# Performance work log

Measured on AMD Instinct MI355X. Metric: run time of the kernel, lower is better.

## Reference

```python
import jax, jax.numpy as jnp
import numpy as np

N = 100000      # nodes
E = 1600000     # edges (before self-loops)
F_IN = 256      # input features
H = 8           # heads, layer 1
FH = 8          # features per head, layer 1
C = 64          # n_classes (layer 2 out, heads=1)
SLOPE = 0.2     # leaky relu negative slope


def setup_inputs() -> dict:
    key = jax.random.key(0)
    ks = jax.random.split(key, 12)
    x = jax.random.normal(ks[0], (N, F_IN), jnp.float32)
    edge_index = jax.random.randint(ks[1], (2, E), 0, N, dtype=jnp.int32)
    # scalar edge weights in [0.5, 1.5) so the (1 - 1/w) correction is well-behaved
    edge_weight = jax.random.uniform(ks[2], (E,), jnp.float32, 0.5, 1.5)
    W1 = jax.random.normal(ks[3], (F_IN, H * FH), jnp.float32) / np.sqrt(F_IN)
    att_src1 = jax.random.normal(ks[4], (H, FH), jnp.float32) * 0.1
    att_dst1 = jax.random.normal(ks[5], (H, FH), jnp.float32) * 0.1
    b1 = jnp.zeros((H * FH,), jnp.float32)
    W2 = jax.random.normal(ks[6], (H * FH, C), jnp.float32) / np.sqrt(H * FH)
    att_src2 = jax.random.normal(ks[7], (1, C), jnp.float32) * 0.1
    att_dst2 = jax.random.normal(ks[8], (1, C), jnp.float32) * 0.1
    b2 = jnp.zeros((C,), jnp.float32)
    return {"x": x, "edge_index": edge_index, "edge_weight": edge_weight,
            "W1": W1, "att_src1": att_src1, "att_dst1": att_dst1, "b1": b1,
            "W2": W2, "att_src2": att_src2, "att_dst2": att_dst2, "b2": b2}


def _gat_layer(x, src, dst, ew, W, a_src, a_dst, b, heads, fph, concat):
    n = x.shape[0]
    h = (x @ W).reshape(n, heads, fph)                      # [N,H,F]
    al_src = jnp.sum(h * a_src, axis=-1)                    # [N,H]
    al_dst = jnp.sum(h * a_dst, axis=-1)                    # [N,H]
    alpha = jax.nn.leaky_relu(al_src[src] + al_dst[dst], SLOPE)  # [E,H]
    alpha = alpha + (1.0 - 1.0 / ew)[:, None]               # scalar edge-weight correction
    # segment softmax over destination nodes
    m = jax.ops.segment_max(alpha, dst, num_segments=n)
    e = jnp.exp(alpha - m[dst])
    s = jax.ops.segment_sum(e, dst, num_segments=n)
    alpha = e / (s[dst] + 1e-16)                            # [E,H]
    msg = h[src] * alpha[:, :, None]                        # [E,H,F]
    out = jax.ops.segment_sum(msg, dst, num_segments=n)     # [N,H,F]
    out = out.reshape(n, heads * fph) if concat else out.mean(axis=1)
    return out + b


def reference(x, edge_index, edge_weight, W1, att_src1, att_dst1, b1,
              W2, att_src2, att_dst2, b2):
    n = x.shape[0]
    loops = jnp.arange(n, dtype=edge_index.dtype)
    src = jnp.concatenate([edge_index[0], loops])
    dst = jnp.concatenate([edge_index[1], loops])
    ew = jnp.concatenate([edge_weight, jnp.ones((n,), edge_weight.dtype)])  # fill_value=1.0
    # dropout layers are identity in eval mode
    h = _gat_layer(x, src, dst, ew, W1, att_src1, att_dst1, b1, H, FH, concat=True)
    h = jax.nn.elu(h)
    out = _gat_layer(h, src, dst, ew, W2, att_src2, att_dst2, b2, 1, C, concat=False)
    return out
```

## Files before the change

kernel.cpp:

```cpp
#include <hip/hip_runtime.h>
#include <math.h>

#define NNODES 100000
#define NEDGES 1600000
#define EATOT  1700000
#define FIN    256
#define C1     64
#define NH     8
#define C2     64
#define SLOPE  0.2f
#define LOG2E  1.4426950408889634f
#define QSCALE 8192.0f

#define NBKT  391
#define BCAP  5120
#define EPB_A 4096
#define NBLK_A 416

#define NT1 3125
#define NT2 1563
#define GGRID 512

typedef __attribute__((ext_vector_type(8))) short short8;
typedef __attribute__((ext_vector_type(4))) float f32x4;

__device__ __forceinline__ unsigned short f2bf(float f){
  unsigned u = __float_as_uint(f);
  unsigned r = (u + 0x7FFFu + ((u >> 16) & 1u)) >> 16;
  return (unsigned short)r;
}

__device__ __forceinline__ void splitw_body(const float* __restrict__ W,
                                            short* __restrict__ th, short* __restrict__ tl,
                                            int K, int idx){
  int k = idx >> 6, c = idx & 63;
  float w = W[idx];
  unsigned int b = __float_as_uint(w);
  unsigned short h = (unsigned short)(b >> 16);
  float hf = __uint_as_float(b & 0xffff0000u);
  float rem = w - hf;
  unsigned short lo = (unsigned short)(__float_as_uint(rem) >> 16);
  th[c * K + k] = (short)h;
  tl[c * K + k] = (short)lo;
}

__global__ void k_pre(const float* __restrict__ W1, short* __restrict__ w1h,
                      short* __restrict__ w1l, const float* __restrict__ W2,
                      short* __restrict__ w2h, short* __restrict__ w2l,
                      int* __restrict__ gcount){
  int b = blockIdx.x, t = threadIdx.x;
  if (b < 64){
    splitw_body(W1, w1h, w1l, FIN, b * 256 + t);
  } else if (b < 80){
    splitw_body(W2, w2h, w2l, C1, (b - 64) * 256 + t);
  } else {
    for (int i = t; i < NBKT; i += 256) gcount[i] = 0;
  }
}

__global__ __launch_bounds__(256) void k_bucketA(
    const int* __restrict__ ei, const float* __restrict__ ew,
    int* __restrict__ gcount, uint2* __restrict__ brec){
  __shared__ int cnt[NBKT];
  __shared__ int base[NBKT];
  int t = threadIdx.x;
  for (int i = t; i < NBKT; i += 256) cnt[i] = 0;
  __syncthreads();
  int e0 = blockIdx.x * EPB_A;
  int e1 = e0 + EPB_A; if (e1 > EATOT) e1 = EATOT;

  int dv[16]; unsigned pv[16];
  #pragma unroll
  for (int i = 0; i < 16; ++i){
    int e = e0 + t + i * 256;
    dv[i] = -1;
    if (e < e1){
      int s, d; float corr;
      if (e < NEDGES){ s = ei[e]; d = ei[NEDGES + e]; corr = 1.0f - 1.0f / ew[e]; }
      else { s = e - NEDGES; d = s; corr = 0.0f; }
      int q = __float2int_rn(corr * (LOG2E * QSCALE));
      dv[i] = d;
      pv[i] = ((unsigned)q << 17) | (unsigned)s;
      atomicAdd(&cnt[d >> 8], 1);
    }
  }
  __syncthreads();
  for (int i = t; i < NBKT; i += 256){
    int c = cnt[i];
    base[i] = c ? atomicAdd(&gcount[i], c) : 0;
    cnt[i] = 0;
  }
  __syncthreads();
  #pragma unroll
  for (int i = 0; i < 16; ++i){
    if (dv[i] >= 0){
      int bkt = dv[i] >> 8;
      int rel = base[bkt] + atomicAdd(&cnt[bkt], 1);
      brec[(size_t)bkt * BCAP + rel] = make_uint2((unsigned)dv[i], pv[i]);
    }
  }
}

__global__ void k_bucketS(const int* __restrict__ gcount, int* __restrict__ gbase,
                          int* __restrict__ rowptr){
  __shared__ int sh[512];
  int t = threadIdx.x;
  int v = (t < NBKT) ? gcount[t] : 0;
  sh[t] = v; __syncthreads();
  for (int off = 1; off < 512; off <<= 1){
    int y = (t >= off) ? sh[t - off] : 0;
    __syncthreads();
    sh[t] += y;
    __syncthreads();
  }
  if (t < NBKT) gbase[t] = sh[t] - v;
  if (t == 0) rowptr[NNODES] = EATOT;
}

__global__ __launch_bounds__(256, 2) void k_bg1(
    const uint2* __restrict__ brec, const int* __restrict__ gcount,
    const int* __restrict__ gbase, int* __restrict__ rowptr, int* __restrict__ rec,
    const float* __restrict__ X, const short* __restrict__ Bth,
    const short* __restrict__ Btl, const float* __restrict__ asrc,
    const float* __restrict__ adst, unsigned short* __restrict__ Hout,
    float* __restrict__ alsrc, float* __restrict__ aldst)
{
  __shared__ float xbuf[2][32 * 256];

  if (blockIdx.x < NBKT){
    int* hist  = (int*)&xbuf[0][0];
    int* scanb = hist + 256;
    int* excl  = scanb + 256;
    int* cur   = excl + 256;
    int bkt = blockIdx.x;
    int t = threadIdx.x;
    int n0 = bkt << 8;
    int cnt = gcount[bkt];
    int gb = gbase[bkt];
    hist[t] = 0;
    __syncthreads();
    const uint2* breg = brec + (size_t)bkt * BCAP;
    for (int j = t; j < cnt; j += 256)
      atomicAdd(&hist[breg[j].x & 255u], 1);
    __syncthreads();
    int h = hist[t];
    scanb[t] = h;
    __syncthreads();
    for (int off = 1; off < 256; off <<= 1){
      int y = (t >= off) ? scanb[t - off] : 0;
      __syncthreads();
      scanb[t] += y;
      __syncthreads();
    }
    int ex = scanb[t] - h;
    excl[t] = ex;
    cur[t] = 0;
    if (n0 + t < NNODES) rowptr[n0 + t] = gb + ex;
    __syncthreads();
    for (int j = t; j < cnt; j += 256){
      uint2 r = breg[j];
      int dl = (int)(r.x & 255u);
      int pos = gb + excl[dl] + atomicAdd(&cur[dl], 1);
      rec[pos] = (int)r.y;
    }
    return;
  }

  const int lane = threadIdx.x & 63;
  const int wave = threadIdx.x >> 6;
  const int l15 = lane & 15;
  const int kg = lane >> 4;
  const int cp = wave & 1;
  const int rh = wave >> 1;
  const int rl = rh * 16 + l15;
  const int rs = rl & 7;

  short8 bh[8][2], bl[8][2];
  #pragma unroll
  for (int ks = 0; ks < 8; ++ks){
    #pragma unroll
    for (int cc = 0; cc < 2; ++cc){
      unsigned boff = (unsigned)((cp * 2 + cc) * 16 + l15) * FIN + ks * 32 + kg * 8;
      bh[ks][cc] = *(const short8*)&Bth[boff];
      bl[ks][cc] = *(const short8*)&Btl[boff];
    }
  }
  float ascv[2], adcv[2];
  #pragma unroll
  for (int cc = 0; cc < 2; ++cc){
    ascv[cc] = asrc[(cp * 2 + cc) * 16 + l15] * LOG2E;
    adcv[cc] = adst[(cp * 2 + cc) * 16 + l15] * LOG2E;
  }

  const int t0 = blockIdx.x - NBKT;
  #pragma unroll
  for (int t = 0; t < 8; ++t){
    int r = wave * 8 + t;
    unsigned u = (unsigned)(lane ^ (r & 7));
    __builtin_amdgcn_global_load_lds(
        (const unsigned int*)(X + (size_t)(t0 * 32 + r) * FIN + u * 4),
        (unsigned int*)&xbuf[0][r * 256], 16, 0, 0);
  }

  int cur = 0;
  for (int ti = t0; ti < NT1; ti += GGRID){
    __syncthreads();
    int nxt = ti + GGRID;
    if (nxt < NT1){
      #pragma unroll
      for (int t = 0; t < 8; ++t){
        int r = wave * 8 + t;
        unsigned u = (unsigned)(lane ^ (r & 7));
        __builtin_amdgcn_global_load_lds(
            (const unsigned int*)(X + (size_t)(nxt * 32 + r) * FIN + u * 4),
            (unsigned int*)&xbuf[cur ^ 1][r * 256], 16, 0, 0);
      }
    }

    f32x4 acc[2] = {f32x4{0,0,0,0}, f32x4{0,0,0,0}};
    #pragma unroll
    for (int ks = 0; ks < 8; ++ks){
      int k0 = ks * 32 + kg * 8;
      unsigned U = (unsigned)(k0 >> 2);
      float4 xa = *(const float4*)&xbuf[cur][rl * 256 + ((U ^ rs) << 2)];
      float4 xb = *(const float4*)&xbuf[cur][rl * 256 + (((U + 1) ^ rs) << 2)];
      float xs[8] = {xa.x, xa.y, xa.z, xa.w, xb.x, xb.y, xb.z, xb.w};
      short8 ah, al;
      #pragma unroll
      for (int j = 0; j < 8; ++j){
        unsigned u = __float_as_uint(xs[j]);
        ah[j] = (short)(u >> 16);
        float hf = __uint_as_float(u & 0xffff0000u);
        al[j] = (short)(__float_as_uint(xs[j] - hf) >> 16);
      }
      #pragma unroll
      for (int cc = 0; cc < 2; ++cc){
        acc[cc] = __builtin_amdgcn_mfma_f32_16x16x32_bf16(ah, bh[ks][cc], acc[cc], 0, 0, 0);
        acc[cc] = __builtin_amdgcn_mfma_f32_16x16x32_bf16(ah, bl[ks][cc], acc[cc], 0, 0, 0);
        acc[cc] = __builtin_amdgcn_mfma_f32_16x16x32_bf16(al, bh[ks][cc], acc[cc], 0, 0, 0);
      }
    }

    int rowg = ti * 32 + rh * 16 + kg * 4;
    #pragma unroll
    for (int cc = 0; cc < 2; ++cc){
      #pragma unroll
      for (int reg = 0; reg < 4; ++reg)
        Hout[(size_t)(rowg + reg) * 64 + (cp * 2 + cc) * 16 + l15] = f2bf(acc[cc][reg]);
    }
    #pragma unroll
    for (int reg = 0; reg < 4; ++reg){
      int r = rowg + reg;
      #pragma unroll
      for (int cc = 0; cc < 2; ++cc){
        float ps = acc[cc][reg] * ascv[cc];
        float pd = acc[cc][reg] * adcv[cc];
        ps += __shfl_xor(ps, 1, 64); ps += __shfl_xor(ps, 2, 64); ps += __shfl_xor(ps, 4, 64);
        pd += __shfl_xor(pd, 1, 64); pd += __shfl_xor(pd, 2, 64); pd += __shfl_xor(pd, 4, 64);
        if ((l15 & 7) == 0){
          int head = (cp * 2 + cc) * 2 + (l15 >> 3);
          alsrc[r * NH + head] = ps;
          aldst[r * NH + head] = pd;
        }
      }
    }
    cur ^= 1;
  }
}

__global__ __launch_bounds__(256, 2) void k_gemm2(
    const unsigned short* __restrict__ Ah, const unsigned short* __restrict__ Al,
    const short* __restrict__ Bth, const short* __restrict__ Btl,
    const float* __restrict__ asrc, const float* __restrict__ adst,
    unsigned short* __restrict__ Hout, float* __restrict__ alsrc,
    float* __restrict__ aldst)
{
  __shared__ unsigned short abuf[2][2][64 * 64];
  const int lane = threadIdx.x & 63;
  const int wave = threadIdx.x >> 6;
  const int l15 = lane & 15;
  const int kg = lane >> 4;
  const int rl = wave * 16 + l15;
  const int rs = rl & 7;

  short8 bh[2][4], bl[2][4];
  #pragma unroll
  for (int ks = 0; ks < 2; ++ks){
    #pragma unroll
    for (int c = 0; c < 4; ++c){
      unsigned boff = (unsigned)(c * 16 + l15) * C1 + ks * 32 + kg * 8;
      bh[ks][c] = *(const short8*)&Bth[boff];
      bl[ks][c] = *(const short8*)&Btl[boff];
    }
  }
  float ascv[4], adcv[4];
  #pragma unroll
  for (int c = 0; c < 4; ++c){
    ascv[c] = asrc[c * 16 + l15] * LOG2E;
    adcv[c] = adst[c * 16 + l15] * LOG2E;
  }

  const int t0 = blockIdx.x;
  auto stage = [&](int buf, int tile){
    #pragma unroll
    for (int j = 0; j < 4; ++j){
      int q = wave * 4 + j;
      int p = q >> 3, rb = q & 7;
      int r = rb * 8 + (lane >> 3);
      int rg = tile * 64 + r; if (rg > NNODES - 1) rg = NNODES - 1;
      unsigned u = (unsigned)((lane & 7) ^ (lane >> 3));
      const unsigned short* src = (p ? Al : Ah) + (size_t)rg * 64 + u * 8;
      __builtin_amdgcn_global_load_lds(
          (const unsigned int*)src,
          (unsigned int*)&abuf[buf][p][rb * 512], 16, 0, 0);
    }
  };
  stage(0, t0);

  int cur = 0;
  for (int ti = t0; ti < NT2; ti += GGRID){
    __syncthreads();
    int nxt = ti + GGRID;
    if (nxt < NT2) stage(cur ^ 1, nxt);

    f32x4 acc[4] = {f32x4{0,0,0,0}, f32x4{0,0,0,0}, f32x4{0,0,0,0}, f32x4{0,0,0,0}};
    #pragma unroll
    for (int ks = 0; ks < 2; ++ks){
      unsigned U = (unsigned)(ks * 4 + kg);
      short8 ah = *(const short8*)&abuf[cur][0][rl * 64 + ((U ^ rs) << 3)];
      short8 al = *(const short8*)&abuf[cur][1][rl * 64 + ((U ^ rs) << 3)];
      #pragma unroll
      for (int c = 0; c < 4; ++c){
        acc[c] = __builtin_amdgcn_mfma_f32_16x16x32_bf16(ah, bh[ks][c], acc[c], 0, 0, 0);
        acc[c] = __builtin_amdgcn_mfma_f32_16x16x32_bf16(ah, bl[ks][c], acc[c], 0, 0, 0);
        acc[c] = __builtin_amdgcn_mfma_f32_16x16x32_bf16(al, bh[ks][c], acc[c], 0, 0, 0);
      }
    }

    int rowg = ti * 64 + wave * 16 + kg * 4;
    #pragma unroll
    for (int c = 0; c < 4; ++c){
      #pragma unroll
      for (int reg = 0; reg < 4; ++reg){
        int r = rowg + reg;
        if (r < NNODES) Hout[(size_t)r * 64 + c * 16 + l15] = f2bf(acc[c][reg]);
      }
    }
    #pragma unroll
    for (int reg = 0; reg < 4; ++reg){
      int r = rowg + reg;
      float ps = 0.0f, pd = 0.0f;
      #pragma unroll
      for (int c = 0; c < 4; ++c){
        ps = fmaf(acc[c][reg], ascv[c], ps);
        pd = fmaf(acc[c][reg], adcv[c], pd);
      }
      ps += __shfl_xor(ps, 1, 64); ps += __shfl_xor(ps, 2, 64);
      ps += __shfl_xor(ps, 4, 64); ps += __shfl_xor(ps, 8, 64);
      pd += __shfl_xor(pd, 1, 64); pd += __shfl_xor(pd, 2, 64);
      pd += __shfl_xor(pd, 4, 64); pd += __shfl_xor(pd, 8, 64);
      if (l15 == 0 && r < NNODES){ alsrc[r] = ps; aldst[r] = pd; }
    }
    cur ^= 1;
  }
}

template<int HEADS, bool DO_ELU, bool SPLIT_OUT>
__global__ __launch_bounds__(256) void k_agg(
    const int* __restrict__ rec, const int* __restrict__ rowptr,
    const unsigned short* __restrict__ hbuf,
    const float* __restrict__ alsrc, const float* __restrict__ aldst,
    const float* __restrict__ bias, float* __restrict__ outF,
    unsigned short* __restrict__ outH, unsigned short* __restrict__ outL){
  __shared__ uint2 wLds[4][2][64];
  int tid = blockIdx.x * blockDim.x + threadIdx.x;
  int dn = tid >> 6;
  int lane = threadIdx.x & 63;
  int w4 = (threadIdx.x >> 6) & 3;
  if (dn >= NNODES) return;
  int d = __builtin_amdgcn_readfirstlane(dn);
  int beg = rowptr[d], end = rowptr[d + 1];
  const int c = lane;
  const int hc = (HEADS == 8) ? (c >> 3) : 0;
  const int eslot = lane >> 3;
  const int hw = (HEADS == 8) ? (lane & 7) : 0;
  const unsigned cOff = (unsigned)c * 2;
  float ad_w = aldst[(size_t)d * HEADS + hw];
  float s = 0.0f, acc = 0.0f;

  auto weight_phase = [&](int j0, int slot){
    int je = j0 + eslot;
    bool valid = (je < end);
    int w = rec[valid ? je : (end - 1)];
    unsigned src = (unsigned)w & 0x1FFFFu;
    float a = alsrc[src * HEADS + hw];
    float v = a + ad_w;
    v = fmaxf(v, v * SLOPE);
    v += (float)(w >> 17) * (1.0f / QSCALE);
    v = fminf(v, 60.0f);
    float e = valid ? __builtin_amdgcn_exp2f(v) : 0.0f;
    wLds[w4][slot][lane] = make_uint2(__float_as_uint(e), src << 7);
  };

  weight_phase(beg, 0);
  int buf = 0;
  for (int j0 = beg; j0 < end; j0 += 8){
    uint2 wv[8];
    #pragma unroll
    for (int i = 0; i < 8; ++i)
      wv[i] = wLds[w4][buf][i * 8 + hc];
    float hv[8];
    #pragma unroll
    for (int i = 0; i < 8; ++i){
      unsigned short raw = *(const unsigned short*)((const char*)hbuf + wv[i].y + cOff);
      hv[i] = __uint_as_float((unsigned)raw << 16);
    }
    int jn = j0 + 8;
    if (jn < end) weight_phase(jn, buf ^ 1);
    #pragma unroll
    for (int i = 0; i < 8; ++i){
      float ev = __uint_as_float(wv[i].x);
      s += ev;
      acc = fmaf(ev, hv[i], acc);
    }
    buf ^= 1;
  }

  float o = acc / (s + 1e-16f) + bias[c];
  if (DO_ELU) o = (o > 0.0f) ? o : (__expf(o) - 1.0f);
  if (SPLIT_OUT){
    unsigned u = __float_as_uint(o);
    outH[(size_t)d * 64 + c] = (unsigned short)(u >> 16);
    float hf = __uint_as_float(u & 0xffff0000u);
    outL[(size_t)d * 64 + c] = (unsigned short)(__float_as_uint(o - hf) >> 16);
  } else {
    outF[(size_t)d * 64 + c] = o;
  }
}

extern "C" void kernel_launch(void* const* d_in, const int* in_sizes, int n_in,
                              void* d_out, int out_size, void* d_ws, size_t ws_size,
                              hipStream_t stream) {
  const float* x    = (const float*)d_in[0];
  const int*   ei   = (const int*)d_in[1];
  const float* ew   = (const float*)d_in[2];
  const float* W1   = (const float*)d_in[3];
  const float* as1  = (const float*)d_in[4];
  const float* ad1  = (const float*)d_in[5];
  const float* b1   = (const float*)d_in[6];
  const float* W2   = (const float*)d_in[7];
  const float* as2  = (const float*)d_in[8];
  const float* ad2  = (const float*)d_in[9];
  const float* b2   = (const float*)d_in[10];
  float* dout = (float*)d_out;

  float* ws = (float*)d_ws;
  size_t off = 0;
  auto alloc = [&](size_t nfloats) -> float* {
    float* p = ws + off;
    off += (nfloats + 15) & ~(size_t)15;
    return p;
  };
  unsigned short* h1 = (unsigned short*)alloc((size_t)NNODES * C1 / 2);
  unsigned short* o1h = (unsigned short*)alloc((size_t)NNODES * C1 / 2);
  unsigned short* o1l = (unsigned short*)alloc((size_t)NNODES * C1 / 2);
  float* alsrc1  = alloc((size_t)NNODES * NH);
  float* aldst1  = alloc((size_t)NNODES * NH);
  float* alsrc2  = alloc(NNODES);
  float* aldst2  = alloc(NNODES);
  int*   gcount  = (int*)alloc(NBKT + 16);
  int*   gbase   = (int*)alloc(NBKT + 16);
  int*   rowptr  = (int*)alloc(NNODES + 1);
  int*   rec     = (int*)alloc(EATOT);
  uint2* brec    = (uint2*)alloc((size_t)NBKT * BCAP * 2);
  short* wt1h    = (short*)alloc(64 * FIN / 2);
  short* wt1l    = (short*)alloc(64 * FIN / 2);
  short* wt2h    = (short*)alloc(64 * C1 / 2);
  short* wt2l    = (short*)alloc(64 * C1 / 2);
  unsigned short* h2 = h1;

  const int BS = 256;

  hipLaunchKernelGGL(k_pre, dim3(81), dim3(BS), 0, stream,
                     W1, wt1h, wt1l, W2, wt2h, wt2l, gcount);

  hipLaunchKernelGGL(k_bucketA, dim3(NBLK_A), dim3(BS), 0, stream, ei, ew, gcount, brec);
  hipLaunchKernelGGL(k_bucketS, dim3(1), dim3(512), 0, stream, gcount, gbase, rowptr);

  hipLaunchKernelGGL(k_bg1, dim3(NBKT + GGRID), dim3(BS), 0, stream,
                     brec, gcount, gbase, rowptr, rec,
                     x, wt1h, wt1l, as1, ad1, h1, alsrc1, aldst1);

  int agrid = (NNODES * 64 + BS - 1) / BS;

  hipLaunchKernelGGL((k_agg<NH, true, true>), dim3(agrid), dim3(BS), 0, stream,
                     rec, rowptr, h1, alsrc1, aldst1, b1, (float*)nullptr, o1h, o1l);

  hipLaunchKernelGGL(k_gemm2, dim3(GGRID), dim3(BS), 0, stream,
                     o1h, o1l, wt2h, wt2l, as2, ad2, h2, alsrc2, aldst2);
  hipLaunchKernelGGL((k_agg<1, false, false>), dim3(agrid), dim3(BS), 0, stream,
                     rec, rowptr, h2, alsrc2, aldst2, b2, dout,
                     (unsigned short*)nullptr, (unsigned short*)nullptr);
}
```

Measured before the change: 199.7 us.

## Shrink k_bg1 GEMM tile to 16 rows and double occupancy and grid

The layer-1 GEMM part of the fused bucket/GEMM kernel now works on 16-row tiles instead of 32. Each wave owns one 16-column slice, so it keeps half as many B fragments in registers, and the LDS staging buffer is halved. Launch bounds rise to 4 blocks per CU and the GEMM grid doubles to 1024 blocks. The aim is more occupancy and better latency hiding for the X stream, at the cost of X being re-read by each wave per column slice from LDS with less reuse per block, plus more tile iterations and barriers.

```diff
diff --git a/kernel.cpp b/kernel.cpp
--- a/kernel.cpp
+++ b/kernel.cpp
@@ -17,7 +17,8 @@
 #define EPB_A 4096
 #define NBLK_A 416
 
-#define NT1 3125
+#define NT1 6250
+#define G1GRID 1024
 #define NT2 1563
 #define GGRID 512
 
@@ -117,7 +118,7 @@
   if (t == 0) rowptr[NNODES] = EATOT;
 }
 
-__global__ __launch_bounds__(256, 2) void k_bg1(
+__global__ __launch_bounds__(256, 4) void k_bg1(
     const uint2* __restrict__ brec, const int* __restrict__ gcount,
     const int* __restrict__ gbase, int* __restrict__ rowptr, int* __restrict__ rec,
     const float* __restrict__ X, const short* __restrict__ Bth,
@@ -125,7 +126,7 @@
     const float* __restrict__ adst, unsigned short* __restrict__ Hout,
     float* __restrict__ alsrc, float* __restrict__ aldst)
 {
-  __shared__ float xbuf[2][32 * 256];
+  __shared__ float xbuf[2][16 * 256];
 
   if (blockIdx.x < NBKT){
     int* hist  = (int*)&xbuf[0][0];
@@ -170,60 +171,44 @@
   const int wave = threadIdx.x >> 6;
   const int l15 = lane & 15;
   const int kg = lane >> 4;
-  const int cp = wave & 1;
-  const int rh = wave >> 1;
-  const int rl = rh * 16 + l15;
-  const int rs = rl & 7;
-
-  short8 bh[8][2], bl[8][2];
+  const int rs = l15 & 7;
+
+  short8 bh[8], bl[8];
   #pragma unroll
   for (int ks = 0; ks < 8; ++ks){
-    #pragma unroll
-    for (int cc = 0; cc < 2; ++cc){
-      unsigned boff = (unsigned)((cp * 2 + cc) * 16 + l15) * FIN + ks * 32 + kg * 8;
-      bh[ks][cc] = *(const short8*)&Bth[boff];
-      bl[ks][cc] = *(const short8*)&Btl[boff];
-    }
-  }
-  float ascv[2], adcv[2];
-  #pragma unroll
-  for (int cc = 0; cc < 2; ++cc){
-    ascv[cc] = asrc[(cp * 2 + cc) * 16 + l15] * LOG2E;
-    adcv[cc] = adst[(cp * 2 + cc) * 16 + l15] * LOG2E;
-  }
+    unsigned boff = (unsigned)(wave * 16 + l15) * FIN + ks * 32 + kg * 8;
+    bh[ks] = *(const short8*)&Bth[boff];
+    bl[ks] = *(const short8*)&Btl[boff];
+  }
+  float ascv = asrc[wave * 16 + l15] * LOG2E;
+  float adcv = adst[wave * 16 + l15] * LOG2E;
 
   const int t0 = blockIdx.x - NBKT;
-  #pragma unroll
-  for (int t = 0; t < 8; ++t){
-    int r = wave * 8 + t;
-    unsigned u = (unsigned)(lane ^ (r & 7));
-    __builtin_amdgcn_global_load_lds(
-        (const unsigned int*)(X + (size_t)(t0 * 32 + r) * FIN + u * 4),
-        (unsigned int*)&xbuf[0][r * 256], 16, 0, 0);
-  }
+  auto stage = [&](int buf, int tile){
+    #pragma unroll
+    for (int t = 0; t < 4; ++t){
+      int r = wave * 4 + t;
+      unsigned u = (unsigned)(lane ^ (r & 7));
+      __builtin_amdgcn_global_load_lds(
+          (const unsigned int*)(X + (size_t)(tile * 16 + r) * FIN + u * 4),
+          (unsigned int*)&xbuf[buf][r * 256], 16, 0, 0);
+    }
+  };
+  stage(0, t0);
 
   int cur = 0;
-  for (int ti = t0; ti < NT1; ti += GGRID){
-    __syncthreads();
-    int nxt = ti + GGRID;
-    if (nxt < NT1){
-      #pragma unroll
-      for (int t = 0; t < 8; ++t){
-        int r = wave * 8 + t;
-        unsigned u = (unsigned)(lane ^ (r & 7));
-        __builtin_amdgcn_global_load_lds(
-            (const unsigned int*)(X + (size_t)(nxt * 32 + r) * FIN + u * 4),
-            (unsigned int*)&xbuf[cur ^ 1][r * 256], 16, 0, 0);
-      }
-    }
-
-    f32x4 acc[2] = {f32x4{0,0,0,0}, f32x4{0,0,0,0}};
+  for (int ti = t0; ti < NT1; ti += G1GRID){
+    __syncthreads();
+    int nxt = ti + G1GRID;
+    if (nxt < NT1) stage(cur ^ 1, nxt);
+
+    f32x4 acc = {0, 0, 0, 0};
     #pragma unroll
     for (int ks = 0; ks < 8; ++ks){
       int k0 = ks * 32 + kg * 8;
       unsigned U = (unsigned)(k0 >> 2);
-      float4 xa = *(const float4*)&xbuf[cur][rl * 256 + ((U ^ rs) << 2)];
-      float4 xb = *(const float4*)&xbuf[cur][rl * 256 + (((U + 1) ^ rs) << 2)];
+      float4 xa = *(const float4*)&xbuf[cur][l15 * 256 + ((U ^ rs) << 2)];
+      float4 xb = *(const float4*)&xbuf[cur][l15 * 256 + (((U + 1) ^ rs) << 2)];
       float xs[8] = {xa.x, xa.y, xa.z, xa.w, xb.x, xb.y, xb.z, xb.w};
       short8 ah, al;
       #pragma unroll
@@ -233,35 +218,26 @@
         float hf = __uint_as_float(u & 0xffff0000u);
         al[j] = (short)(__float_as_uint(xs[j] - hf) >> 16);
       }
-      #pragma unroll
-      for (int cc = 0; cc < 2; ++cc){
-        acc[cc] = __builtin_amdgcn_mfma_f32_16x16x32_bf16(ah, bh[ks][cc], acc[cc], 0, 0, 0);
-        acc[cc] = __builtin_amdgcn_mfma_f32_16x16x32_bf16(ah, bl[ks][cc], acc[cc], 0, 0, 0);
-        acc[cc] = __builtin_amdgcn_mfma_f32_16x16x32_bf16(al, bh[ks][cc], acc[cc], 0, 0, 0);
-      }
-    }
-
-    int rowg = ti * 32 + rh * 16 + kg * 4;
-    #pragma unroll
-    for (int cc = 0; cc < 2; ++cc){
-      #pragma unroll
-      for (int reg = 0; reg < 4; ++reg)
-        Hout[(size_t)(rowg + reg) * 64 + (cp * 2 + cc) * 16 + l15] = f2bf(acc[cc][reg]);
-    }
+      acc = __builtin_amdgcn_mfma_f32_16x16x32_bf16(ah, bh[ks], acc, 0, 0, 0);
+      acc = __builtin_amdgcn_mfma_f32_16x16x32_bf16(ah, bl[ks], acc, 0, 0, 0);
+      acc = __builtin_amdgcn_mfma_f32_16x16x32_bf16(al, bh[ks], acc, 0, 0, 0);
+    }
+
+    int rowg = ti * 16 + kg * 4;
+    #pragma unroll
+    for (int reg = 0; reg < 4; ++reg)
+      Hout[(size_t)(rowg + reg) * 64 + wave * 16 + l15] = f2bf(acc[reg]);
     #pragma unroll
     for (int reg = 0; reg < 4; ++reg){
       int r = rowg + reg;
-      #pragma unroll
-      for (int cc = 0; cc < 2; ++cc){
-        float ps = acc[cc][reg] * ascv[cc];
-        float pd = acc[cc][reg] * adcv[cc];
-        ps += __shfl_xor(ps, 1, 64); ps += __shfl_xor(ps, 2, 64); ps += __shfl_xor(ps, 4, 64);
-        pd += __shfl_xor(pd, 1, 64); pd += __shfl_xor(pd, 2, 64); pd += __shfl_xor(pd, 4, 64);
-        if ((l15 & 7) == 0){
-          int head = (cp * 2 + cc) * 2 + (l15 >> 3);
-          alsrc[r * NH + head] = ps;
-          aldst[r * NH + head] = pd;
-        }
+      float ps = acc[reg] * ascv;
+      float pd = acc[reg] * adcv;
+      ps += __shfl_xor(ps, 1, 64); ps += __shfl_xor(ps, 2, 64); ps += __shfl_xor(ps, 4, 64);
+      pd += __shfl_xor(pd, 1, 64); pd += __shfl_xor(pd, 2, 64); pd += __shfl_xor(pd, 4, 64);
+      if ((l15 & 7) == 0){
+        int head = wave * 2 + (l15 >> 3);
+        alsrc[r * NH + head] = ps;
+        aldst[r * NH + head] = pd;
       }
     }
     cur ^= 1;
@@ -487,7 +463,7 @@
   hipLaunchKernelGGL(k_bucketA, dim3(NBLK_A), dim3(BS), 0, stream, ei, ew, gcount, brec);
   hipLaunchKernelGGL(k_bucketS, dim3(1), dim3(512), 0, stream, gcount, gbase, rowptr);
 
-  hipLaunchKernelGGL(k_bg1, dim3(NBKT + GGRID), dim3(BS), 0, stream,
+  hipLaunchKernelGGL(k_bg1, dim3(NBKT + G1GRID), dim3(BS), 0, stream,
                      brec, gcount, gbase, rowptr, rec,
                      x, wt1h, wt1l, as1, ad1, h1, alsrc1, aldst1);
 
```

Measured after the change: 200.1 us. Within noise of the previous version (+0.2%).
